# Kernel optimization log

Hardware: AMD Instinct MI355X
Metric: run time of the kernel (lower is better)

Reference implementation:

```python
import jax
import jax.numpy as jnp
from jax import lax
import numpy as np

B, C, H, W = 32, 256, 64, 64
R = 16  # low-rank dim of random bias


def setup_inputs() -> dict:
    key = jax.random.key(0)
    ks = jax.random.split(key, 6)
    return {
        "x": jax.random.normal(ks[0], (B, C, H, W), dtype=jnp.float32),
        "x_mid": jax.random.normal(ks[1], (B, C, H, W), dtype=jnp.float32),
        "g_w": jax.random.normal(ks[2], (C, C, 3, 3), dtype=jnp.float32) * 0.02,
        "w_w": jax.random.normal(ks[3], (C, C, 1, 1), dtype=jnp.float32) * 0.02,
        "weight1": jax.random.normal(ks[4], (C, R), dtype=jnp.float32) * 0.1,
        "weight2": jax.random.normal(ks[5], (C, R), dtype=jnp.float32) * 0.1,
    }


def _conv(x, w, padding):
    return lax.conv_general_dilated(
        x, w, window_strides=(1, 1), padding=padding,
        dimension_numbers=("NCHW", "OIHW", "NCHW"))


def reference(x, x_mid, g_w, w_w, weight1, weight2):
    b, c, h, w = x.shape
    # value path: 3x3 conv on x_mid (padding 1 -> SAME)
    g_x = _conv(x_mid, g_w, "SAME")                       # [b,c,h,w]
    value = g_x.reshape(b, c, h * w)                       # [b,c,N]
    feats = x.reshape(b, c, h * w)                         # query == key == x
    # channel-channel similarity: [b,c,c]
    sim = jnp.einsum("bcn,bdn->bcd", feats, feats) * (c ** -0.5)
    random_map = weight1 @ weight2.T                        # [c,c] low-rank bias
    attn = jax.nn.softmax(sim + random_map[None, :, :], axis=-1)
    context = jnp.einsum("bcd,bdn->bcn", attn, value).reshape(b, c, h, w)
    return _conv(context, w_w, "VALID")                     # 1x1 conv
```

## Files before the change

kernel.cpp:

```cpp
#include <hip/hip_runtime.h>


#define NB 32
#define NC 256
#define NPIX 4096

typedef __attribute__((ext_vector_type(8))) short short8;
typedef __attribute__((ext_vector_type(16))) float floatx16;

__device__ inline short f2bf(float f) {
    union { float f; unsigned u; } v; v.f = f;
    unsigned r = v.u + 0x7fffu + ((v.u >> 16) & 1u);
    return (short)(r >> 16);
}

__global__ __launch_bounds__(256) void rm_kernel(const float* __restrict__ w1,
                                                 const float* __restrict__ w2,
                                                 float* __restrict__ rm) {
    int idx = blockIdx.x * 256 + threadIdx.x;
    int c = idx >> 8, d = idx & 255;
    float s = 0.f;
#pragma unroll
    for (int r = 0; r < 16; r++) s += w1[c * 16 + r] * w2[d * 16 + r];
    rm[idx] = s;
}

__global__ __launch_bounds__(256) void cvt_bf16_kernel(const float* __restrict__ in,
                                                       short* __restrict__ out) {
    size_t i = ((size_t)blockIdx.x * 256 + threadIdx.x) * 8;
    float4 v0 = *(const float4*)&in[i];
    float4 v1 = *(const float4*)&in[i + 4];
    short8 s;
    s[0] = f2bf(v0.x); s[1] = f2bf(v0.y); s[2] = f2bf(v0.z); s[3] = f2bf(v0.w);
    s[4] = f2bf(v1.x); s[5] = f2bf(v1.y); s[6] = f2bf(v1.z); s[7] = f2bf(v1.w);
    *(short8*)&out[i] = s;
}

__global__ __launch_bounds__(256) void cvt_x_kernel(const float* __restrict__ x,
                                                    short* __restrict__ xt) {
    const int h = blockIdx.x;
    const int b = blockIdx.y;
    __shared__ short xls[64 * 256];
    const int tid = threadIdx.x;
    for (int i = tid; i < 4096; i += 256) {
        int ci = i >> 4, w4 = (i & 15) << 2;
        float4 v = *(const float4*)&x[(((size_t)(b * 256 + ci)) * 64 + h) * 64 + w4];
        xls[(w4 + 0) * 256 + ci] = f2bf(v.x);
        xls[(w4 + 1) * 256 + ci] = f2bf(v.y);
        xls[(w4 + 2) * 256 + ci] = f2bf(v.z);
        xls[(w4 + 3) * 256 + ci] = f2bf(v.w);
    }
    __syncthreads();
    uint4* dst = (uint4*)&xt[(((size_t)(b * 64 + h)) * 64) * 256];
    const uint4* src = (const uint4*)xls;
    for (int i = tid; i < 2048; i += 256) dst[i] = src[i];
}

__global__ __launch_bounds__(256) void cvt_w_kernel(const float* __restrict__ g_w,
                                                    short* __restrict__ wt) {
    int o = blockIdx.x * 256 + threadIdx.x;
    if (o >= 73728) return;
    int co_t = o / 18432;
    int rem  = o - co_t * 18432;
    int ci_b = rem / 1152;
    int rem2 = rem - ci_b * 1152;
    int tap  = rem2 / 128;
    int rem3 = rem2 - tap * 128;
    int ch   = rem3 >> 6, ls = rem3 & 63;
    int co = co_t * 64 + ch * 32 + (ls & 31);
    int ci0 = ci_b * 16 + (ls >> 5) * 8;
    short8 v;
#pragma unroll
    for (int j = 0; j < 8; j++)
        v[j] = f2bf(g_w[((size_t)co * 256 + ci0 + j) * 9 + tap]);
    *(short8*)&wt[(size_t)o * 8] = v;
}

__global__ __launch_bounds__(256) void conv_mfma(const short* __restrict__ xt,
                                                 const short* __restrict__ wt,
                                                 short* __restrict__ value_t) {
    const int h0  = blockIdx.x * 4;
    const int cot = blockIdx.y;
    const int b   = blockIdx.z;
    __shared__ short ws[9 * 2 * 64 * 8];
    __shared__ short xs[6 * 2 * 66 * 8];
    const int tid = threadIdx.x;
    const int wv = tid >> 6, lane = tid & 63;
    const int kh2 = lane >> 5, ln = lane & 31;

    floatx16 acc00 = {}, acc01 = {}, acc10 = {}, acc11 = {};

    for (int cib = 0; cib < 16; ++cib) {
        __syncthreads();
        {
            const uint4* src = (const uint4*)&wt[((size_t)(cot * 16 + cib) * 1152) * 8];
            uint4* dst = (uint4*)ws;
            for (int i = tid; i < 1152; i += 256) dst[i] = src[i];
        }
        {
            uint4* dst = (uint4*)xs;
            for (int i = tid; i < 792; i += 256) {
                if (i < 768) {
                    int r = i >> 7, rem = i & 127, w = rem >> 1, half = rem & 1;
                    int hin = h0 - 1 + r;
                    uint4 v = make_uint4(0, 0, 0, 0);
                    if ((unsigned)hin < 64u)
                        v = *(const uint4*)&xt[(((size_t)(b * 64 + hin)) * 64 + w) * 256 + cib * 16 + half * 8];
                    dst[(r * 2 + half) * 66 + 1 + w] = v;
                } else {
                    int j = i - 768;
                    int r = j >> 2, half = (j >> 1) & 1, side = j & 1;
                    dst[(r * 2 + half) * 66 + side * 65] = make_uint4(0, 0, 0, 0);
                }
            }
        }
        __syncthreads();

#pragma unroll
        for (int tap = 0; tap < 9; ++tap) {
            const int kh = tap / 3, kw = tap - kh * 3;
            const int r = wv + kh;
            short8 wf0 = *(const short8*)&ws[((tap * 2 + 0) * 64 + lane) * 8];
            short8 wf1 = *(const short8*)&ws[((tap * 2 + 1) * 64 + lane) * 8];
            short8 xf0 = *(const short8*)&xs[(((r * 2 + kh2) * 66) + kw + ln) * 8];
            short8 xf1 = *(const short8*)&xs[(((r * 2 + kh2) * 66) + kw + 32 + ln) * 8];
            acc00 = __builtin_amdgcn_mfma_f32_32x32x16_bf16(xf0, wf0, acc00, 0, 0, 0);
            acc01 = __builtin_amdgcn_mfma_f32_32x32x16_bf16(xf0, wf1, acc01, 0, 0, 0);
            acc10 = __builtin_amdgcn_mfma_f32_32x32x16_bf16(xf1, wf0, acc10, 0, 0, 0);
            acc11 = __builtin_amdgcn_mfma_f32_32x32x16_bf16(xf1, wf1, acc11, 0, 0, 0);
        }
    }

    const int h_out = h0 + wv;
    short* vt = value_t + ((size_t)(b * 4096 + h_out * 64)) * 256 + cot * 64;
#pragma unroll
    for (int reg = 0; reg < 16; ++reg) {
        int m = (reg & 3) + 8 * (reg >> 2) + 4 * kh2;
        vt[(size_t)m * 256 + ln]             = f2bf(acc00[reg]);
        vt[(size_t)m * 256 + 32 + ln]        = f2bf(acc01[reg]);
        vt[(size_t)(m + 32) * 256 + ln]      = f2bf(acc10[reg]);
        vt[(size_t)(m + 32) * 256 + 32 + ln] = f2bf(acc11[reg]);
    }
}

__global__ __launch_bounds__(128) void gemm_nt_bf16(const short* __restrict__ A,
                                                    const short* __restrict__ B,
                                                    float* __restrict__ C, int K,
                                                    long sA, long sB, long sC,
                                                    int ldc, int tilesN) {
    const int mt = blockIdx.x / tilesN, nt = blockIdx.x % tilesN;
    A += (size_t)blockIdx.y * sA;
    B += (size_t)blockIdx.y * sB;
    C += (size_t)blockIdx.y * sC;
    const int wv = threadIdx.x >> 6, l = threadIdx.x & 63;
    const int ln = l & 31, kh = l >> 5;
    const short* arow = A + (size_t)(mt * 64 + wv * 32 + ln) * K + kh * 8;
    const short* brow = B + (size_t)(nt * 128 + ln) * K + kh * 8;
    floatx16 acc0 = {}, acc1 = {}, acc2 = {}, acc3 = {};
#pragma unroll 2
    for (int k0 = 0; k0 < K; k0 += 16) {
        short8 a  = *(const short8*)&arow[k0];
        short8 b0 = *(const short8*)&brow[k0];
        short8 b1 = *(const short8*)&brow[(size_t)32 * K + k0];
        short8 b2 = *(const short8*)&brow[(size_t)64 * K + k0];
        short8 b3 = *(const short8*)&brow[(size_t)96 * K + k0];
        acc0 = __builtin_amdgcn_mfma_f32_32x32x16_bf16(a, b0, acc0, 0, 0, 0);
        acc1 = __builtin_amdgcn_mfma_f32_32x32x16_bf16(a, b1, acc1, 0, 0, 0);
        acc2 = __builtin_amdgcn_mfma_f32_32x32x16_bf16(a, b2, acc2, 0, 0, 0);
        acc3 = __builtin_amdgcn_mfma_f32_32x32x16_bf16(a, b3, acc3, 0, 0, 0);
    }
    const int n0 = nt * 128;
#pragma unroll
    for (int reg = 0; reg < 16; ++reg) {
        int m = mt * 64 + wv * 32 + (reg & 3) + 8 * (reg >> 2) + 4 * kh;
        float* crow = C + (size_t)m * ldc + n0 + ln;
        crow[0]  = acc0[reg];
        crow[32] = acc1[reg];
        crow[64] = acc2[reg];
        crow[96] = acc3[reg];
    }
}

template <int BT, int OB>
__global__ __launch_bounds__(256) void gemm64(const float* __restrict__ A,
                                              const float* __restrict__ B,
                                              float* __restrict__ C, int K,
                                              long sA, long sB, long sC,
                                              int ldA, int ldB, int ldC, int tilesN) {
    const int m0 = (blockIdx.x / tilesN) * 64;
    const int n0 = (blockIdx.x % tilesN) * 64;
    A += (size_t)blockIdx.y * sA;
    B += (size_t)blockIdx.y * sB;
    const size_t coff = (size_t)blockIdx.y * sC;
    __shared__ float As[16][68], Bs[16][68];
    const int tid = threadIdx.x;
    const int tx = tid & 15, ty = tid >> 4;
    const int mm = tid >> 2, kk4 = (tid & 3) * 4;
    float acc[4][4] = {};

    for (int k0 = 0; k0 < K; k0 += 16) {
        __syncthreads();
        {
            float4 a = *(const float4*)&A[(size_t)(m0 + mm) * ldA + k0 + kk4];
            As[kk4 + 0][mm] = a.x; As[kk4 + 1][mm] = a.y;
            As[kk4 + 2][mm] = a.z; As[kk4 + 3][mm] = a.w;
        }
        if (BT) {
            float4 bv = *(const float4*)&B[(size_t)(n0 + mm) * ldB + k0 + kk4];
            Bs[kk4 + 0][mm] = bv.x; Bs[kk4 + 1][mm] = bv.y;
            Bs[kk4 + 2][mm] = bv.z; Bs[kk4 + 3][mm] = bv.w;
        } else {
            int bk = tid >> 4, bn = (tid & 15) * 4;
            *(float4*)&Bs[bk][bn] = *(const float4*)&B[(size_t)(k0 + bk) * ldB + n0 + bn];
        }
        __syncthreads();
#pragma unroll
        for (int kk = 0; kk < 16; kk++) {
            float4 a = *(float4*)&As[kk][ty * 4];
            float4 bv = *(float4*)&Bs[kk][tx * 4];
            float av[4] = {a.x, a.y, a.z, a.w};
            float bb[4] = {bv.x, bv.y, bv.z, bv.w};
#pragma unroll
            for (int i = 0; i < 4; i++)
#pragma unroll
                for (int j = 0; j < 4; j++) acc[i][j] += av[i] * bb[j];
        }
    }
#pragma unroll
    for (int i = 0; i < 4; i++) {
        if (OB) {
            short* Cs = (short*)C + coff;
            short4 o;
            o.x = f2bf(acc[i][0]); o.y = f2bf(acc[i][1]);
            o.z = f2bf(acc[i][2]); o.w = f2bf(acc[i][3]);
            *(short4*)&Cs[(size_t)(m0 + ty * 4 + i) * ldC + n0 + tx * 4] = o;
        } else {
            float* Cf = (float*)C + coff;
            float4 o = make_float4(acc[i][0], acc[i][1], acc[i][2], acc[i][3]);
            *(float4*)&Cf[(size_t)(m0 + ty * 4 + i) * ldC + n0 + tx * 4] = o;
        }
    }
}

__global__ __launch_bounds__(256) void softmax_kernel(float* __restrict__ sim,
                                                      const float* __restrict__ rm) {
    int row  = blockIdx.x * 4 + (threadIdx.x >> 6);
    int lane = threadIdx.x & 63;
    int c = row & 255;
    float4 v = *(float4*)&sim[(size_t)row * 256 + lane * 4];
    const float4 bias = *(const float4*)&rm[c * 256 + lane * 4];
    v.x = v.x * 0.0625f + bias.x;
    v.y = v.y * 0.0625f + bias.y;
    v.z = v.z * 0.0625f + bias.z;
    v.w = v.w * 0.0625f + bias.w;
    float m = fmaxf(fmaxf(v.x, v.y), fmaxf(v.z, v.w));
#pragma unroll
    for (int off = 32; off > 0; off >>= 1) m = fmaxf(m, __shfl_xor(m, off, 64));
    float e0 = __expf(v.x - m), e1 = __expf(v.y - m);
    float e2 = __expf(v.z - m), e3 = __expf(v.w - m);
    float s = e0 + e1 + e2 + e3;
#pragma unroll
    for (int off = 32; off > 0; off >>= 1) s += __shfl_xor(s, off, 64);
    float inv = 1.f / s;
    float4 o = make_float4(e0 * inv, e1 * inv, e2 * inv, e3 * inv);
    *(float4*)&sim[(size_t)row * 256 + lane * 4] = o;
}

extern "C" void kernel_launch(void* const* d_in, const int* in_sizes, int n_in,
                              void* d_out, int out_size, void* d_ws, size_t ws_size,
                              hipStream_t stream) {
    const float* x     = (const float*)d_in[0];
    const float* x_mid = (const float*)d_in[1];
    const float* g_w   = (const float*)d_in[2];
    const float* w_w   = (const float*)d_in[3];
    const float* w1    = (const float*)d_in[4];
    const float* w2    = (const float*)d_in[5];
    float* out = (float*)d_out;

    char* ws = (char*)d_ws;
    short* value_t = (short*)ws;
    float* sim     = (float*)(ws + (size_t)NB * NPIX * NC * 2);
    short* attn2_b = (short*)(sim + (size_t)NB * NC * NC);
    float* rm      = (float*)(attn2_b + (size_t)NB * NC * NC);
    short* xt      = (short*)(rm + NC * NC);
    short* xb      = xt + (size_t)NB * NPIX * NC;
    short* wt      = xb + (size_t)NB * NC * NPIX;

    cvt_w_kernel<<<288, 256, 0, stream>>>(g_w, wt);
    cvt_x_kernel<<<dim3(64, 32), 256, 0, stream>>>(x_mid, xt);
    cvt_bf16_kernel<<<16384, 256, 0, stream>>>(x, xb);
    rm_kernel<<<256, 256, 0, stream>>>(w1, w2, rm);
    conv_mfma<<<dim3(16, 4, 32), 256, 0, stream>>>(xt, wt, value_t);
    gemm_nt_bf16<<<dim3(8, 32), 128, 0, stream>>>(
        xb, xb, sim, 4096,
        (long)NC * NPIX, (long)NC * NPIX, (long)NC * NC, NC, 2);
    softmax_kernel<<<2048, 256, 0, stream>>>(sim, rm);
    gemm64<0, 1><<<dim3(16, 32), 256, 0, stream>>>(
        w_w, sim, (float*)attn2_b, 256,
        0L, (long)NC * NC, (long)NC * NC,
        NC, NC, NC, 4);
    gemm_nt_bf16<<<dim3(128, 32), 128, 0, stream>>>(
        attn2_b, value_t, out, 256,
        (long)NC * NC, (long)NPIX * NC, (long)NC * NPIX, NPIX, 32);
}
```

Measured before the change: 730.9 us.

## Split-K the Gram GEMM and register-prefetch conv tiles

Result: faster. 703.8 us (-3.7%).

```diff
diff --git a/kernel.cpp b/kernel.cpp
--- a/kernel.cpp
+++ b/kernel.cpp
@@ -4,6 +4,7 @@
 #define NB 32
 #define NC 256
 #define NPIX 4096
+#define KSPLIT 4
 
 typedef __attribute__((ext_vector_type(8))) short short8;
 typedef __attribute__((ext_vector_type(16))) float floatx16;
@@ -88,32 +89,58 @@
     const int wv = tid >> 6, lane = tid & 63;
     const int kh2 = lane >> 5, ln = lane & 31;
 
+    int xr0, xw0, xh0_, xr1, xw1, xh1_, xr2, xw2, xh2_;
+    {
+        int i0 = tid;        xr0 = i0 >> 7; int r0 = i0 & 127; xw0 = r0 >> 1; xh0_ = r0 & 1;
+        int i1 = tid + 256;  xr1 = i1 >> 7; int r1 = i1 & 127; xw1 = r1 >> 1; xh1_ = r1 & 1;
+        int i2 = tid + 512;  xr2 = i2 >> 7; int r2 = i2 & 127; xw2 = r2 >> 1; xh2_ = r2 & 1;
+    }
+    const int xd0 = (xr0 * 2 + xh0_) * 66 + 1 + xw0;
+    const int xd1 = (xr1 * 2 + xh1_) * 66 + 1 + xw1;
+    const int xd2 = (xr2 * 2 + xh2_) * 66 + 1 + xw2;
+    const int hin0 = h0 - 1 + xr0, hin1 = h0 - 1 + xr1, hin2 = h0 - 1 + xr2;
+    const uint4* wsrc_base = (const uint4*)&wt[(size_t)(cot * 16) * 1152 * 8];
+
+    uint4 wr0, wr1, wr2, wr3, wr4;
+    uint4 xv0, xv1, xv2;
+
+#define LOAD_CIB(c)                                                            \
+    do {                                                                       \
+        const uint4* wsrc = wsrc_base + (size_t)(c) * 1152;                    \
+        wr0 = wsrc[tid];        wr1 = wsrc[tid + 256];                         \
+        wr2 = wsrc[tid + 512];  wr3 = wsrc[tid + 768];                         \
+        if (tid < 128) wr4 = wsrc[tid + 1024];                                 \
+        xv0 = make_uint4(0, 0, 0, 0); xv1 = xv0; xv2 = xv0;                    \
+        if ((unsigned)hin0 < 64u)                                              \
+            xv0 = *(const uint4*)&xt[(((size_t)(b * 64 + hin0)) * 64 + xw0) * 256 + (c) * 16 + xh0_ * 8]; \
+        if ((unsigned)hin1 < 64u)                                              \
+            xv1 = *(const uint4*)&xt[(((size_t)(b * 64 + hin1)) * 64 + xw1) * 256 + (c) * 16 + xh1_ * 8]; \
+        if ((unsigned)hin2 < 64u)                                              \
+            xv2 = *(const uint4*)&xt[(((size_t)(b * 64 + hin2)) * 64 + xw2) * 256 + (c) * 16 + xh2_ * 8]; \
+    } while (0)
+
+#define WRITE_LDS()                                                            \
+    do {                                                                       \
+        uint4* wdst = (uint4*)ws;                                              \
+        wdst[tid] = wr0;        wdst[tid + 256] = wr1;                         \
+        wdst[tid + 512] = wr2;  wdst[tid + 768] = wr3;                         \
+        if (tid < 128) wdst[tid + 1024] = wr4;                                 \
+        uint4* xdst = (uint4*)xs;                                              \
+        xdst[xd0] = xv0; xdst[xd1] = xv1; xdst[xd2] = xv2;                     \
+    } while (0)
+
+    if (tid < 24) {
+        int r = tid >> 2, half = (tid >> 1) & 1, side = tid & 1;
+        ((uint4*)xs)[(r * 2 + half) * 66 + side * 65] = make_uint4(0, 0, 0, 0);
+    }
+
     floatx16 acc00 = {}, acc01 = {}, acc10 = {}, acc11 = {};
 
+    LOAD_CIB(0);
     for (int cib = 0; cib < 16; ++cib) {
         __syncthreads();
-        {
-            const uint4* src = (const uint4*)&wt[((size_t)(cot * 16 + cib) * 1152) * 8];
-            uint4* dst = (uint4*)ws;
-            for (int i = tid; i < 1152; i += 256) dst[i] = src[i];
-        }
-        {
-            uint4* dst = (uint4*)xs;
-            for (int i = tid; i < 792; i += 256) {
-                if (i < 768) {
-                    int r = i >> 7, rem = i & 127, w = rem >> 1, half = rem & 1;
-                    int hin = h0 - 1 + r;
-                    uint4 v = make_uint4(0, 0, 0, 0);
-                    if ((unsigned)hin < 64u)
-                        v = *(const uint4*)&xt[(((size_t)(b * 64 + hin)) * 64 + w) * 256 + cib * 16 + half * 8];
-                    dst[(r * 2 + half) * 66 + 1 + w] = v;
-                } else {
-                    int j = i - 768;
-                    int r = j >> 2, half = (j >> 1) & 1, side = j & 1;
-                    dst[(r * 2 + half) * 66 + side * 65] = make_uint4(0, 0, 0, 0);
-                }
-            }
-        }
+        WRITE_LDS();
+        if (cib < 15) LOAD_CIB(cib + 1);
         __syncthreads();
 
 #pragma unroll
@@ -130,6 +157,8 @@
             acc11 = __builtin_amdgcn_mfma_f32_32x32x16_bf16(xf1, wf1, acc11, 0, 0, 0);
         }
     }
+#undef LOAD_CIB
+#undef WRITE_LDS
 
     const int h_out = h0 + wv;
     short* vt = value_t + ((size_t)(b * 4096 + h_out * 64)) * 256 + cot * 64;
@@ -145,25 +174,30 @@
 
 __global__ __launch_bounds__(128) void gemm_nt_bf16(const short* __restrict__ A,
                                                     const short* __restrict__ B,
-                                                    float* __restrict__ C, int K,
+                                                    float* __restrict__ C,
+                                                    int Kld, int Ksub,
                                                     long sA, long sB, long sC,
-                                                    int ldc, int tilesN) {
-    const int mt = blockIdx.x / tilesN, nt = blockIdx.x % tilesN;
+                                                    int ldc, int tilesN, int tilesXY,
+                                                    long sKsl) {
+    const int kslice = blockIdx.x / tilesXY;
+    const int t = blockIdx.x - kslice * tilesXY;
+    const int mt = t / tilesN, nt = t - (t / tilesN) * tilesN;
     A += (size_t)blockIdx.y * sA;
     B += (size_t)blockIdx.y * sB;
-    C += (size_t)blockIdx.y * sC;
+    C += (size_t)blockIdx.y * sC + (size_t)kslice * sKsl;
     const int wv = threadIdx.x >> 6, l = threadIdx.x & 63;
     const int ln = l & 31, kh = l >> 5;
-    const short* arow = A + (size_t)(mt * 64 + wv * 32 + ln) * K + kh * 8;
-    const short* brow = B + (size_t)(nt * 128 + ln) * K + kh * 8;
+    const int kbase = kslice * Ksub;
+    const short* arow = A + (size_t)(mt * 64 + wv * 32 + ln) * Kld + kbase + kh * 8;
+    const short* brow = B + (size_t)(nt * 128 + ln) * Kld + kbase + kh * 8;
     floatx16 acc0 = {}, acc1 = {}, acc2 = {}, acc3 = {};
 #pragma unroll 2
-    for (int k0 = 0; k0 < K; k0 += 16) {
+    for (int k0 = 0; k0 < Ksub; k0 += 16) {
         short8 a  = *(const short8*)&arow[k0];
         short8 b0 = *(const short8*)&brow[k0];
-        short8 b1 = *(const short8*)&brow[(size_t)32 * K + k0];
-        short8 b2 = *(const short8*)&brow[(size_t)64 * K + k0];
-        short8 b3 = *(const short8*)&brow[(size_t)96 * K + k0];
+        short8 b1 = *(const short8*)&brow[(size_t)32 * Kld + k0];
+        short8 b2 = *(const short8*)&brow[(size_t)64 * Kld + k0];
+        short8 b3 = *(const short8*)&brow[(size_t)96 * Kld + k0];
         acc0 = __builtin_amdgcn_mfma_f32_32x32x16_bf16(a, b0, acc0, 0, 0, 0);
         acc1 = __builtin_amdgcn_mfma_f32_32x32x16_bf16(a, b1, acc1, 0, 0, 0);
         acc2 = __builtin_amdgcn_mfma_f32_32x32x16_bf16(a, b2, acc2, 0, 0, 0);
@@ -243,11 +277,21 @@
 }
 
 __global__ __launch_bounds__(256) void softmax_kernel(float* __restrict__ sim,
+                                                      const float* __restrict__ part,
                                                       const float* __restrict__ rm) {
     int row  = blockIdx.x * 4 + (threadIdx.x >> 6);
     int lane = threadIdx.x & 63;
     int c = row & 255;
-    float4 v = *(float4*)&sim[(size_t)row * 256 + lane * 4];
+    const size_t off = (size_t)row * 256 + lane * 4;
+    const size_t sP = (size_t)NB * NC * NC;
+    float4 v  = *(const float4*)&part[off];
+    float4 p1 = *(const float4*)&part[off + sP];
+    float4 p2 = *(const float4*)&part[off + 2 * sP];
+    float4 p3 = *(const float4*)&part[off + 3 * sP];
+    v.x += p1.x + p2.x + p3.x;
+    v.y += p1.y + p2.y + p3.y;
+    v.z += p1.z + p2.z + p3.z;
+    v.w += p1.w + p2.w + p3.w;
     const float4 bias = *(const float4*)&rm[c * 256 + lane * 4];
     v.x = v.x * 0.0625f + bias.x;
     v.y = v.y * 0.0625f + bias.y;
@@ -255,15 +299,15 @@
     v.w = v.w * 0.0625f + bias.w;
     float m = fmaxf(fmaxf(v.x, v.y), fmaxf(v.z, v.w));
 #pragma unroll
-    for (int off = 32; off > 0; off >>= 1) m = fmaxf(m, __shfl_xor(m, off, 64));
+    for (int off2 = 32; off2 > 0; off2 >>= 1) m = fmaxf(m, __shfl_xor(m, off2, 64));
     float e0 = __expf(v.x - m), e1 = __expf(v.y - m);
     float e2 = __expf(v.z - m), e3 = __expf(v.w - m);
     float s = e0 + e1 + e2 + e3;
 #pragma unroll
-    for (int off = 32; off > 0; off >>= 1) s += __shfl_xor(s, off, 64);
+    for (int off2 = 32; off2 > 0; off2 >>= 1) s += __shfl_xor(s, off2, 64);
     float inv = 1.f / s;
     float4 o = make_float4(e0 * inv, e1 * inv, e2 * inv, e3 * inv);
-    *(float4*)&sim[(size_t)row * 256 + lane * 4] = o;
+    *(float4*)&sim[off] = o;
 }
 
 extern "C" void kernel_launch(void* const* d_in, const int* in_sizes, int n_in,
@@ -286,20 +330,23 @@
     short* xb      = xt + (size_t)NB * NPIX * NC;
     short* wt      = xb + (size_t)NB * NC * NPIX;
 
+    float* simPart = out;
+
     cvt_w_kernel<<<288, 256, 0, stream>>>(g_w, wt);
     cvt_x_kernel<<<dim3(64, 32), 256, 0, stream>>>(x_mid, xt);
     cvt_bf16_kernel<<<16384, 256, 0, stream>>>(x, xb);
     rm_kernel<<<256, 256, 0, stream>>>(w1, w2, rm);
     conv_mfma<<<dim3(16, 4, 32), 256, 0, stream>>>(xt, wt, value_t);
-    gemm_nt_bf16<<<dim3(8, 32), 128, 0, stream>>>(
-        xb, xb, sim, 4096,
-        (long)NC * NPIX, (long)NC * NPIX, (long)NC * NC, NC, 2);
-    softmax_kernel<<<2048, 256, 0, stream>>>(sim, rm);
+    gemm_nt_bf16<<<dim3(8 * KSPLIT, 32), 128, 0, stream>>>(
+        xb, xb, simPart, 4096, 4096 / KSPLIT,
+        (long)NC * NPIX, (long)NC * NPIX, (long)NC * NC, NC, 2, 8,
+        (long)NB * NC * NC);
+    softmax_kernel<<<2048, 256, 0, stream>>>(sim, simPart, rm);
     gemm64<0, 1><<<dim3(16, 32), 256, 0, stream>>>(
         w_w, sim, (float*)attn2_b, 256,
         0L, (long)NC * NC, (long)NC * NC,
         NC, NC, NC, 4);
     gemm_nt_bf16<<<dim3(128, 32), 128, 0, stream>>>(
-        attn2_b, value_t, out, 256,
-        (long)NC * NC, (long)NPIX * NC, (long)NC * NPIX, NPIX, 32);
-}
+        attn2_b, value_t, out, 256, 256,
+        (long)NC * NC, (long)NPIX * NC, (long)NC * NPIX, NPIX, 32, 128, 0L);
+}
```

## Widen conv tile to 128 output channels and prefetch next input-channel block into registers

Applied to the files above, without the earlier changes.

New measurement: 794.3 us. 1.09x slower.

```diff
diff --git a/kernel.cpp b/kernel.cpp
--- a/kernel.cpp
+++ b/kernel.cpp
@@ -79,67 +79,111 @@
 __global__ __launch_bounds__(256) void conv_mfma(const short* __restrict__ xt,
                                                  const short* __restrict__ wt,
                                                  short* __restrict__ value_t) {
-    const int h0  = blockIdx.x * 4;
-    const int cot = blockIdx.y;
-    const int b   = blockIdx.z;
-    __shared__ short ws[9 * 2 * 64 * 8];
+    const int h0 = blockIdx.x * 4;
+    const int cp = blockIdx.y;
+    const int b  = blockIdx.z;
+    __shared__ short ws[2 * 9 * 2 * 64 * 8];
     __shared__ short xs[6 * 2 * 66 * 8];
     const int tid = threadIdx.x;
     const int wv = tid >> 6, lane = tid & 63;
     const int kh2 = lane >> 5, ln = lane & 31;
 
-    floatx16 acc00 = {}, acc01 = {}, acc10 = {}, acc11 = {};
-
+    int xr0, xw0, xh0_, xr1, xw1, xh1_, xr2, xw2, xh2_;
+    {
+        int i0 = tid;        xr0 = i0 >> 7; int r0 = i0 & 127; xw0 = r0 >> 1; xh0_ = r0 & 1;
+        int i1 = tid + 256;  xr1 = i1 >> 7; int r1 = i1 & 127; xw1 = r1 >> 1; xh1_ = r1 & 1;
+        int i2 = tid + 512;  xr2 = i2 >> 7; int r2 = i2 & 127; xw2 = r2 >> 1; xh2_ = r2 & 1;
+    }
+    const int xd0 = (xr0 * 2 + xh0_) * 66 + 1 + xw0;
+    const int xd1 = (xr1 * 2 + xh1_) * 66 + 1 + xw1;
+    const int xd2 = (xr2 * 2 + xh2_) * 66 + 1 + xw2;
+    const int hin0 = h0 - 1 + xr0, hin1 = h0 - 1 + xr1, hin2 = h0 - 1 + xr2;
+
+    const uint4* wbase = (const uint4*)wt;
+    uint wsoff[9];
+#pragma unroll
+    for (int k = 0; k < 9; ++k) {
+        int i = tid + 256 * k;
+        wsoff[k] = (i < 1152) ? (uint)((cp * 2) * 16 * 1152 + i)
+                              : (uint)((cp * 2 + 1) * 16 * 1152 + i - 1152);
+    }
+
+    uint4 wr[9];
+    uint4 xv0, xv1, xv2;
+
+#define LOAD_CIB(c)                                                            \
+    do {                                                                       \
+        _Pragma("unroll")                                                      \
+        for (int k = 0; k < 9; ++k) wr[k] = wbase[wsoff[k] + (c) * 1152];      \
+        xv0 = make_uint4(0, 0, 0, 0); xv1 = xv0; xv2 = xv0;                    \
+        if ((unsigned)hin0 < 64u)                                              \
+            xv0 = *(const uint4*)&xt[(((size_t)(b * 64 + hin0)) * 64 + xw0) * 256 + (c) * 16 + xh0_ * 8]; \
+        if ((unsigned)hin1 < 64u)                                              \
+            xv1 = *(const uint4*)&xt[(((size_t)(b * 64 + hin1)) * 64 + xw1) * 256 + (c) * 16 + xh1_ * 8]; \
+        if ((unsigned)hin2 < 64u)                                              \
+            xv2 = *(const uint4*)&xt[(((size_t)(b * 64 + hin2)) * 64 + xw2) * 256 + (c) * 16 + xh2_ * 8]; \
+    } while (0)
+
+#define WRITE_LDS()                                                            \
+    do {                                                                       \
+        uint4* wdst = (uint4*)ws;                                              \
+        _Pragma("unroll")                                                      \
+        for (int k = 0; k < 9; ++k) wdst[tid + 256 * k] = wr[k];               \
+        uint4* xdst = (uint4*)xs;                                              \
+        xdst[xd0] = xv0; xdst[xd1] = xv1; xdst[xd2] = xv2;                     \
+    } while (0)
+
+    if (tid < 24) {
+        int r = tid >> 2, half = (tid >> 1) & 1, side = tid & 1;
+        ((uint4*)xs)[(r * 2 + half) * 66 + side * 65] = make_uint4(0, 0, 0, 0);
+    }
+
+    floatx16 acc00 = {}, acc01 = {}, acc02 = {}, acc03 = {};
+    floatx16 acc10 = {}, acc11 = {}, acc12 = {}, acc13 = {};
+
+    LOAD_CIB(0);
     for (int cib = 0; cib < 16; ++cib) {
         __syncthreads();
-        {
-            const uint4* src = (const uint4*)&wt[((size_t)(cot * 16 + cib) * 1152) * 8];
-            uint4* dst = (uint4*)ws;
-            for (int i = tid; i < 1152; i += 256) dst[i] = src[i];
-        }
-        {
-            uint4* dst = (uint4*)xs;
-            for (int i = tid; i < 792; i += 256) {
-                if (i < 768) {
-                    int r = i >> 7, rem = i & 127, w = rem >> 1, half = rem & 1;
-                    int hin = h0 - 1 + r;
-                    uint4 v = make_uint4(0, 0, 0, 0);
-                    if ((unsigned)hin < 64u)
-                        v = *(const uint4*)&xt[(((size_t)(b * 64 + hin)) * 64 + w) * 256 + cib * 16 + half * 8];
-                    dst[(r * 2 + half) * 66 + 1 + w] = v;
-                } else {
-                    int j = i - 768;
-                    int r = j >> 2, half = (j >> 1) & 1, side = j & 1;
-                    dst[(r * 2 + half) * 66 + side * 65] = make_uint4(0, 0, 0, 0);
-                }
-            }
-        }
+        WRITE_LDS();
+        if (cib < 15) LOAD_CIB(cib + 1);
         __syncthreads();
 
 #pragma unroll
         for (int tap = 0; tap < 9; ++tap) {
             const int kh = tap / 3, kw = tap - kh * 3;
             const int r = wv + kh;
-            short8 wf0 = *(const short8*)&ws[((tap * 2 + 0) * 64 + lane) * 8];
-            short8 wf1 = *(const short8*)&ws[((tap * 2 + 1) * 64 + lane) * 8];
+            short8 wf00 = *(const short8*)&ws[(((0 * 9 + tap) * 2 + 0) * 64 + lane) * 8];
+            short8 wf01 = *(const short8*)&ws[(((0 * 9 + tap) * 2 + 1) * 64 + lane) * 8];
+            short8 wf10 = *(const short8*)&ws[(((1 * 9 + tap) * 2 + 0) * 64 + lane) * 8];
+            short8 wf11 = *(const short8*)&ws[(((1 * 9 + tap) * 2 + 1) * 64 + lane) * 8];
             short8 xf0 = *(const short8*)&xs[(((r * 2 + kh2) * 66) + kw + ln) * 8];
             short8 xf1 = *(const short8*)&xs[(((r * 2 + kh2) * 66) + kw + 32 + ln) * 8];
-            acc00 = __builtin_amdgcn_mfma_f32_32x32x16_bf16(xf0, wf0, acc00, 0, 0, 0);
-            acc01 = __builtin_amdgcn_mfma_f32_32x32x16_bf16(xf0, wf1, acc01, 0, 0, 0);
-            acc10 = __builtin_amdgcn_mfma_f32_32x32x16_bf16(xf1, wf0, acc10, 0, 0, 0);
-            acc11 = __builtin_amdgcn_mfma_f32_32x32x16_bf16(xf1, wf1, acc11, 0, 0, 0);
-        }
-    }
+            acc00 = __builtin_amdgcn_mfma_f32_32x32x16_bf16(xf0, wf00, acc00, 0, 0, 0);
+            acc01 = __builtin_amdgcn_mfma_f32_32x32x16_bf16(xf0, wf01, acc01, 0, 0, 0);
+            acc02 = __builtin_amdgcn_mfma_f32_32x32x16_bf16(xf0, wf10, acc02, 0, 0, 0);
+            acc03 = __builtin_amdgcn_mfma_f32_32x32x16_bf16(xf0, wf11, acc03, 0, 0, 0);
+            acc10 = __builtin_amdgcn_mfma_f32_32x32x16_bf16(xf1, wf00, acc10, 0, 0, 0);
+            acc11 = __builtin_amdgcn_mfma_f32_32x32x16_bf16(xf1, wf01, acc11, 0, 0, 0);
+            acc12 = __builtin_amdgcn_mfma_f32_32x32x16_bf16(xf1, wf10, acc12, 0, 0, 0);
+            acc13 = __builtin_amdgcn_mfma_f32_32x32x16_bf16(xf1, wf11, acc13, 0, 0, 0);
+        }
+    }
+#undef LOAD_CIB
+#undef WRITE_LDS
 
     const int h_out = h0 + wv;
-    short* vt = value_t + ((size_t)(b * 4096 + h_out * 64)) * 256 + cot * 64;
+    short* vt = value_t + ((size_t)(b * 4096 + h_out * 64)) * 256 + cp * 128;
 #pragma unroll
     for (int reg = 0; reg < 16; ++reg) {
         int m = (reg & 3) + 8 * (reg >> 2) + 4 * kh2;
         vt[(size_t)m * 256 + ln]             = f2bf(acc00[reg]);
         vt[(size_t)m * 256 + 32 + ln]        = f2bf(acc01[reg]);
+        vt[(size_t)m * 256 + 64 + ln]        = f2bf(acc02[reg]);
+        vt[(size_t)m * 256 + 96 + ln]        = f2bf(acc03[reg]);
         vt[(size_t)(m + 32) * 256 + ln]      = f2bf(acc10[reg]);
         vt[(size_t)(m + 32) * 256 + 32 + ln] = f2bf(acc11[reg]);
+        vt[(size_t)(m + 32) * 256 + 64 + ln] = f2bf(acc12[reg]);
+        vt[(size_t)(m + 32) * 256 + 96 + ln] = f2bf(acc13[reg]);
     }
 }
 
@@ -290,7 +334,7 @@
     cvt_x_kernel<<<dim3(64, 32), 256, 0, stream>>>(x_mid, xt);
     cvt_bf16_kernel<<<16384, 256, 0, stream>>>(x, xb);
     rm_kernel<<<256, 256, 0, stream>>>(w1, w2, rm);
-    conv_mfma<<<dim3(16, 4, 32), 256, 0, stream>>>(xt, wt, value_t);
+    conv_mfma<<<dim3(16, 2, 32), 256, 0, stream>>>(xt, wt, value_t);
     gemm_nt_bf16<<<dim3(8, 32), 128, 0, stream>>>(
         xb, xb, sim, 4096,
         (long)NC * NPIX, (long)NC * NPIX, (long)NC * NC, NC, 2);
```

## Double-buffer conv weights via direct LDS loads and prefetch input tiles into registers

Applied to the files above, without the earlier changes.

Measured after the change: 684.4 us. 1.07x faster.

```diff
diff --git a/kernel.cpp b/kernel.cpp
--- a/kernel.cpp
+++ b/kernel.cpp
@@ -7,6 +7,9 @@
 
 typedef __attribute__((ext_vector_type(8))) short short8;
 typedef __attribute__((ext_vector_type(16))) float floatx16;
+
+typedef __attribute__((address_space(1))) const unsigned int guint;
+typedef __attribute__((address_space(3))) unsigned int luint;
 
 __device__ inline short f2bf(float f) {
     union { float f; unsigned u; } v; v.f = f;
@@ -82,46 +85,79 @@
     const int h0  = blockIdx.x * 4;
     const int cot = blockIdx.y;
     const int b   = blockIdx.z;
-    __shared__ short ws[9 * 2 * 64 * 8];
+    __shared__ short ws[2][9 * 2 * 64 * 8];
     __shared__ short xs[6 * 2 * 66 * 8];
     const int tid = threadIdx.x;
     const int wv = tid >> 6, lane = tid & 63;
     const int kh2 = lane >> 5, ln = lane & 31;
 
+    int xr0, xw0, xh0_, xr1, xw1, xh1_, xr2, xw2, xh2_;
+    {
+        int i0 = tid;        xr0 = i0 >> 7; int r0 = i0 & 127; xw0 = r0 >> 1; xh0_ = r0 & 1;
+        int i1 = tid + 256;  xr1 = i1 >> 7; int r1 = i1 & 127; xw1 = r1 >> 1; xh1_ = r1 & 1;
+        int i2 = tid + 512;  xr2 = i2 >> 7; int r2 = i2 & 127; xw2 = r2 >> 1; xh2_ = r2 & 1;
+    }
+    const int xd0 = (xr0 * 2 + xh0_) * 66 + 1 + xw0;
+    const int xd1 = (xr1 * 2 + xh1_) * 66 + 1 + xw1;
+    const int xd2 = (xr2 * 2 + xh2_) * 66 + 1 + xw2;
+    const int hin0 = h0 - 1 + xr0, hin1 = h0 - 1 + xr1, hin2 = h0 - 1 + xr2;
+
+    const short* wsrc0 = wt + (size_t)(cot * 16) * 1152 * 8;
+
+#define STAGE_W(c)                                                             \
+    do {                                                                       \
+        short* wsd = ws[(c) & 1];                                              \
+        const short* wsg = wsrc0 + (size_t)(c) * 1152 * 8;                     \
+        _Pragma("unroll")                                                      \
+        for (int j = 0; j < 5; ++j) {                                          \
+            int k = wv + 4 * j;                                                \
+            if (k < 18)                                                        \
+                __builtin_amdgcn_global_load_lds(                              \
+                    (guint*)(wsg + (size_t)(k * 64 + lane) * 8),               \
+                    (luint*)(wsd + k * 512), 16, 0, 0);                        \
+        }                                                                      \
+    } while (0)
+
+    uint4 xv0, xv1, xv2;
+#define LOAD_X(c)                                                              \
+    do {                                                                       \
+        xv0 = make_uint4(0, 0, 0, 0); xv1 = xv0; xv2 = xv0;                    \
+        if ((unsigned)hin0 < 64u)                                              \
+            xv0 = *(const uint4*)&xt[(((size_t)(b * 64 + hin0)) * 64 + xw0) * 256 + (c) * 16 + xh0_ * 8]; \
+        if ((unsigned)hin1 < 64u)                                              \
+            xv1 = *(const uint4*)&xt[(((size_t)(b * 64 + hin1)) * 64 + xw1) * 256 + (c) * 16 + xh1_ * 8]; \
+        if ((unsigned)hin2 < 64u)                                              \
+            xv2 = *(const uint4*)&xt[(((size_t)(b * 64 + hin2)) * 64 + xw2) * 256 + (c) * 16 + xh2_ * 8]; \
+    } while (0)
+
+    if (tid < 24) {
+        int r = tid >> 2, half = (tid >> 1) & 1, side = tid & 1;
+        ((uint4*)xs)[(r * 2 + half) * 66 + side * 65] = make_uint4(0, 0, 0, 0);
+    }
+
     floatx16 acc00 = {}, acc01 = {}, acc10 = {}, acc11 = {};
 
+    STAGE_W(0);
+    LOAD_X(0);
     for (int cib = 0; cib < 16; ++cib) {
         __syncthreads();
         {
-            const uint4* src = (const uint4*)&wt[((size_t)(cot * 16 + cib) * 1152) * 8];
-            uint4* dst = (uint4*)ws;
-            for (int i = tid; i < 1152; i += 256) dst[i] = src[i];
-        }
-        {
-            uint4* dst = (uint4*)xs;
-            for (int i = tid; i < 792; i += 256) {
-                if (i < 768) {
-                    int r = i >> 7, rem = i & 127, w = rem >> 1, half = rem & 1;
-                    int hin = h0 - 1 + r;
-                    uint4 v = make_uint4(0, 0, 0, 0);
-                    if ((unsigned)hin < 64u)
-                        v = *(const uint4*)&xt[(((size_t)(b * 64 + hin)) * 64 + w) * 256 + cib * 16 + half * 8];
-                    dst[(r * 2 + half) * 66 + 1 + w] = v;
-                } else {
-                    int j = i - 768;
-                    int r = j >> 2, half = (j >> 1) & 1, side = j & 1;
-                    dst[(r * 2 + half) * 66 + side * 65] = make_uint4(0, 0, 0, 0);
-                }
-            }
+            uint4* xdst = (uint4*)xs;
+            xdst[xd0] = xv0; xdst[xd1] = xv1; xdst[xd2] = xv2;
         }
         __syncthreads();
-
+        if (cib < 15) {
+            STAGE_W(cib + 1);
+            LOAD_X(cib + 1);
+        }
+
+        const short* wsc = ws[cib & 1];
 #pragma unroll
         for (int tap = 0; tap < 9; ++tap) {
             const int kh = tap / 3, kw = tap - kh * 3;
             const int r = wv + kh;
-            short8 wf0 = *(const short8*)&ws[((tap * 2 + 0) * 64 + lane) * 8];
-            short8 wf1 = *(const short8*)&ws[((tap * 2 + 1) * 64 + lane) * 8];
+            short8 wf0 = *(const short8*)&wsc[((tap * 2 + 0) * 64 + lane) * 8];
+            short8 wf1 = *(const short8*)&wsc[((tap * 2 + 1) * 64 + lane) * 8];
             short8 xf0 = *(const short8*)&xs[(((r * 2 + kh2) * 66) + kw + ln) * 8];
             short8 xf1 = *(const short8*)&xs[(((r * 2 + kh2) * 66) + kw + 32 + ln) * 8];
             acc00 = __builtin_amdgcn_mfma_f32_32x32x16_bf16(xf0, wf0, acc00, 0, 0, 0);
@@ -130,6 +166,8 @@
             acc11 = __builtin_amdgcn_mfma_f32_32x32x16_bf16(xf1, wf1, acc11, 0, 0, 0);
         }
     }
+#undef LOAD_X
+#undef STAGE_W
 
     const int h_out = h0 + wv;
     short* vt = value_t + ((size_t)(b * 4096 + h_out * 64)) * 256 + cot * 64;
```
